# Kernel tuning notes

Measured on AMD Instinct MI355X. Metric: run time of the kernel, lower is better.

Reference implementation:

```python
import jax, jax.numpy as jnp
import numpy as np

B, S, D, H, DH, F = 2, 2048, 768, 12, 64, 3072
EPS = 1e-5


def setup_inputs() -> dict:
    key = jax.random.key(0)
    ks = jax.random.split(key, 12)
    sd = 0.02
    return {
        "x":   jax.random.normal(ks[0], (B, S, D), jnp.float32),
        "Wq":  jax.random.normal(ks[1], (H, D, DH), jnp.float32) * sd,
        "bq":  jnp.zeros((H, DH), jnp.float32),
        "Wk":  jax.random.normal(ks[2], (H, D, DH), jnp.float32) * sd,
        "bk":  jnp.zeros((H, DH), jnp.float32),
        "Wv":  jax.random.normal(ks[3], (H, D, DH), jnp.float32) * sd,
        "bv":  jnp.zeros((H, DH), jnp.float32),
        "Wo":  jax.random.normal(ks[4], (H * DH, D), jnp.float32) * sd,
        "bo":  jnp.zeros((D,), jnp.float32),
        "g1":  jnp.ones((D,), jnp.float32),
        "be1": jnp.zeros((D,), jnp.float32),
        "W1":  jax.random.normal(ks[5], (D, F), jnp.float32) * sd,
        "b1":  jnp.zeros((F,), jnp.float32),
        "W2":  jax.random.normal(ks[6], (F, D), jnp.float32) * sd,
        "b2":  jnp.zeros((D,), jnp.float32),
        "g2":  jnp.ones((D,), jnp.float32),
        "be2": jnp.zeros((D,), jnp.float32),
    }


def _layer_norm(x, g, b):
    mu = jnp.mean(x, axis=-1, keepdims=True)
    var = jnp.mean(jnp.square(x - mu), axis=-1, keepdims=True)
    return (x - mu) * jax.lax.rsqrt(var + EPS) * g + b


def reference(x, Wq, bq, Wk, bk, Wv, bv, Wo, bo, g1, be1, W1, b1, W2, b2, g2, be2):
    # per-head projections (vectorized over heads); eval mode: dropout = identity
    q = jnp.einsum('bsd,hde->bhse', x, Wq) + bq[:, None, :]   # [B,H,S,DH]
    k = jnp.einsum('bsd,hde->bhse', x, Wk) + bk[:, None, :]
    v = jnp.einsum('bsd,hde->bhse', x, Wv) + bv[:, None, :]
    scale = jnp.asarray(DH ** 0.5, x.dtype)
    scores = jnp.einsum('bhse,bhte->bhst', q, k) / scale      # [B,H,S,S]
    attn = jax.nn.softmax(scores, axis=-1)
    ctx = jnp.einsum('bhst,bhte->bhse', attn, v)              # [B,H,S,DH]
    # concat heads (head-major order matches torch.cat over head list)
    concat = jnp.transpose(ctx, (0, 2, 1, 3)).reshape(x.shape[0], x.shape[1], H * DH)
    attn_out = concat @ Wo + bo
    x1 = _layer_norm(x + attn_out, g1, be1)
    ff = jax.nn.relu(x1 @ W1 + b1) @ W2 + b2
    return _layer_norm(x1 + ff, g2, be2)
```

## Files before the change

kernel.cpp:

```cpp
#include <hip/hip_runtime.h>
#include <hip/hip_bf16.h>

typedef __attribute__((ext_vector_type(8))) short short8;
typedef __attribute__((ext_vector_type(4))) float f32x4;

constexpr int Bb  = 2;
constexpr int Ss  = 2048;
constexpr int Dd  = 768;
constexpr int Hh  = 12;
constexpr int DHh = 64;
constexpr int Ff  = 3072;
constexpr int Mr  = Bb * Ss;
constexpr int QKVN = 3 * Hh * DHh;

__device__ __forceinline__ unsigned short f2bf(float f) {
    union { float f; unsigned u; } x{f};
    unsigned r = x.u + 0x7fffu + ((x.u >> 16) & 1u);
    return (unsigned short)(r >> 16);
}

__device__ __forceinline__ int swz(int row, int cbyte) {
    return row * 128 + (cbyte ^ ((row & 7) << 4));
}

__device__ __forceinline__ void gload16(const void* g, void* l) {
    __builtin_amdgcn_global_load_lds(
        (const __attribute__((address_space(1))) unsigned int*)g,
        (__attribute__((address_space(3))) unsigned int*)l, 16, 0, 0);
}

__global__ __launch_bounds__(256) void cast_bf16(const float* __restrict__ in,
                                                 unsigned short* __restrict__ out, int n) {
    int i = (blockIdx.x * 256 + threadIdx.x) * 4;
    if (i >= n) return;
    float4 v = *(const float4*)(in + i);
    ushort4 o;
    o.x = f2bf(v.x); o.y = f2bf(v.y); o.z = f2bf(v.z); o.w = f2bf(v.w);
    *(ushort4*)(out + i) = o;
}

__global__ __launch_bounds__(256) void pack_b(const float* __restrict__ bq,
                                              const float* __restrict__ bk,
                                              const float* __restrict__ bv,
                                              float* __restrict__ bpack) {
    int c = blockIdx.x * 256 + threadIdx.x;
    if (c >= QKVN) return;
    const float* bsrc = (c < 768) ? bq : (c < 1536) ? bk : bv;
    float v = bsrc[c % 768];
    bpack[c] = (c < 768) ? v * 0.125f : v;
}

__global__ __launch_bounds__(256) void transpose_cast_t(const float* __restrict__ W,
                                                        unsigned short* __restrict__ WT,
                                                        int K, int N) {
    __shared__ float t[64][65];
    const int k0 = blockIdx.y * 64, n0 = blockIdx.x * 64;
    const int tid = threadIdx.x;
    const int r = tid >> 4, c4 = (tid & 15) * 4;
#pragma unroll
    for (int i = 0; i < 4; ++i) {
        float4 v = *(const float4*)&W[(size_t)(k0 + r + i * 16) * N + n0 + c4];
        t[r + i * 16][c4 + 0] = v.x;
        t[r + i * 16][c4 + 1] = v.y;
        t[r + i * 16][c4 + 2] = v.z;
        t[r + i * 16][c4 + 3] = v.w;
    }
    __syncthreads();
#pragma unroll
    for (int i = 0; i < 4; ++i) {
        int n = r + i * 16;
        ushort4 o;
        o.x = f2bf(t[c4 + 0][n]);
        o.y = f2bf(t[c4 + 1][n]);
        o.z = f2bf(t[c4 + 2][n]);
        o.w = f2bf(t[c4 + 3][n]);
        *(ushort4*)&WT[(size_t)(n0 + n) * K + k0 + c4] = o;
    }
}

__global__ __launch_bounds__(256) void pack_wqkvT_t(const float* __restrict__ Wq,
                                                    const float* __restrict__ Wk,
                                                    const float* __restrict__ Wv,
                                                    unsigned short* __restrict__ WT) {
    __shared__ float t[64][65];
    const int sh = blockIdx.z;
    const int s = sh / Hh, h = sh % Hh;
    const float* W = ((s == 0) ? Wq : (s == 1) ? Wk : Wv) + (size_t)h * Dd * DHh;
    const float scale = (s == 0) ? 0.125f : 1.0f;
    const int d0 = blockIdx.x * 64;
    const int tid = threadIdx.x;
    const int r = tid >> 4, c4 = (tid & 15) * 4;
#pragma unroll
    for (int i = 0; i < 4; ++i) {
        float4 v = *(const float4*)&W[(size_t)(d0 + r + i * 16) * DHh + c4];
        t[r + i * 16][c4 + 0] = v.x * scale;
        t[r + i * 16][c4 + 1] = v.y * scale;
        t[r + i * 16][c4 + 2] = v.z * scale;
        t[r + i * 16][c4 + 3] = v.w * scale;
    }
    __syncthreads();
    const size_t nbase = (size_t)s * 768 + h * 64;
#pragma unroll
    for (int i = 0; i < 4; ++i) {
        int e = r + i * 16;
        ushort4 o;
        o.x = f2bf(t[c4 + 0][e]);
        o.y = f2bf(t[c4 + 1][e]);
        o.z = f2bf(t[c4 + 2][e]);
        o.w = f2bf(t[c4 + 3][e]);
        *(ushort4*)&WT[(nbase + e) * Dd + d0 + c4] = o;
    }
}

__global__ __launch_bounds__(256) void vtrans(const unsigned short* __restrict__ qkvb,
                                              unsigned short* __restrict__ vT) {
    __shared__ unsigned short t[64][72];
    const int bh = blockIdx.y, b = bh / Hh, h = bh % Hh;
    const int s0 = blockIdx.x * 64;
    const int tid = threadIdx.x;
    for (int i = 0; i < 2; ++i) {
        int slot = i * 256 + tid;
        int r = slot >> 3, c8 = (slot & 7) * 8;
        uint4 v = *(const uint4*)(qkvb + (size_t)(b * Ss + s0 + r) * QKVN + 1536 + h * 64 + c8);
        *(uint4*)&t[r][c8] = v;
    }
    __syncthreads();
    for (int i = 0; i < 2; ++i) {
        int slot = i * 256 + tid;
        int d = slot >> 3, c8 = (slot & 7) * 8;
        alignas(16) unsigned short tmp[8];
#pragma unroll
        for (int j = 0; j < 8; ++j) tmp[j] = t[c8 + j][d];
        *(uint4*)(vT + ((size_t)bh * DHh + d) * Ss + s0 + c8) = *(const uint4*)tmp;
    }
}

template <int OUT_BF16, int RELU>
__global__ __launch_bounds__(256) void gemm_bf16(const unsigned short* __restrict__ A,
                                                 const unsigned short* __restrict__ BT,
                                                 const float* __restrict__ bias,
                                                 void* __restrict__ Cv,
                                                 int M, int N, int K) {
    __shared__ unsigned short As[128 * 32];
    __shared__ unsigned short Bs[128 * 32];
    const int tid = threadIdx.x;
    const int row0 = blockIdx.y * 128, col0 = blockIdx.x * 128;
    const int lane = tid & 63, w = tid >> 6;
    const int wr = w >> 1, wc = w & 1;

    const int ar0 = tid >> 2,         ac0 = (tid & 3) * 8;
    const int ar1 = (tid + 256) >> 2, ac1 = ((tid + 256) & 3) * 8;

    const int kfrag = (lane >> 4) * 8;
    const int rA = wr * 64 + (lane & 15);
    const int rB = wc * 64 + (lane & 15);

    f32x4 acc[4][4] = {};

    for (int k0 = 0; k0 < K; k0 += 32) {
        gload16(&A [(size_t)(row0 + ar0) * K + k0 + ac0], &As[ar0 * 32 + ac0]);
        gload16(&A [(size_t)(row0 + ar1) * K + k0 + ac1], &As[ar1 * 32 + ac1]);
        gload16(&BT[(size_t)(col0 + ar0) * K + k0 + ac0], &Bs[ar0 * 32 + ac0]);
        gload16(&BT[(size_t)(col0 + ar1) * K + k0 + ac1], &Bs[ar1 * 32 + ac1]);
        __syncthreads();

        short8 a[4], b[4];
#pragma unroll
        for (int i = 0; i < 4; ++i) {
            a[i] = *(const short8*)&As[(rA + i * 16) * 32 + kfrag];
            b[i] = *(const short8*)&Bs[(rB + i * 16) * 32 + kfrag];
        }
#pragma unroll
        for (int mi = 0; mi < 4; ++mi)
#pragma unroll
            for (int ni = 0; ni < 4; ++ni)
                acc[mi][ni] = __builtin_amdgcn_mfma_f32_16x16x32_bf16(a[mi], b[ni], acc[mi][ni], 0, 0, 0);
        __syncthreads();
    }

    const int crow = (lane >> 4) * 4, ccol = lane & 15;
#pragma unroll
    for (int mi = 0; mi < 4; ++mi) {
#pragma unroll
        for (int ni = 0; ni < 4; ++ni) {
            const int c = col0 + wc * 64 + ni * 16 + ccol;
            const float bv = bias[c];
#pragma unroll
            for (int j = 0; j < 4; ++j) {
                const int r = row0 + wr * 64 + mi * 16 + crow + j;
                float val = acc[mi][ni][j] + bv;
                if (RELU) val = fmaxf(val, 0.f);
                if (OUT_BF16)
                    ((unsigned short*)Cv)[(size_t)r * N + c] = f2bf(val);
                else
                    ((float*)Cv)[(size_t)r * N + c] = val;
            }
        }
    }
}

__global__ __launch_bounds__(256) void gemm_splitk(const unsigned short* __restrict__ A,
                                                   const unsigned short* __restrict__ BT,
                                                   unsigned short* __restrict__ part,
                                                   int M, int N, int KC, int LD) {
    __shared__ unsigned short As[128 * 32];
    __shared__ unsigned short Bs[128 * 32];
    const int s = blockIdx.z;
    A    += (size_t)s * KC;
    BT   += (size_t)s * KC;
    part += (size_t)s * M * N;

    const int tid = threadIdx.x;
    const int row0 = blockIdx.y * 128, col0 = blockIdx.x * 128;
    const int lane = tid & 63, w = tid >> 6;
    const int wr = w >> 1, wc = w & 1;

    const int ar0 = tid >> 2,         ac0 = (tid & 3) * 8;
    const int ar1 = (tid + 256) >> 2, ac1 = ((tid + 256) & 3) * 8;

    const int kfrag = (lane >> 4) * 8;
    const int rA = wr * 64 + (lane & 15);
    const int rB = wc * 64 + (lane & 15);

    f32x4 acc[4][4] = {};

    for (int k0 = 0; k0 < KC; k0 += 32) {
        gload16(&A [(size_t)(row0 + ar0) * LD + k0 + ac0], &As[ar0 * 32 + ac0]);
        gload16(&A [(size_t)(row0 + ar1) * LD + k0 + ac1], &As[ar1 * 32 + ac1]);
        gload16(&BT[(size_t)(col0 + ar0) * LD + k0 + ac0], &Bs[ar0 * 32 + ac0]);
        gload16(&BT[(size_t)(col0 + ar1) * LD + k0 + ac1], &Bs[ar1 * 32 + ac1]);
        __syncthreads();

        short8 a[4], b[4];
#pragma unroll
        for (int i = 0; i < 4; ++i) {
            a[i] = *(const short8*)&As[(rA + i * 16) * 32 + kfrag];
            b[i] = *(const short8*)&Bs[(rB + i * 16) * 32 + kfrag];
        }
#pragma unroll
        for (int mi = 0; mi < 4; ++mi)
#pragma unroll
            for (int ni = 0; ni < 4; ++ni)
                acc[mi][ni] = __builtin_amdgcn_mfma_f32_16x16x32_bf16(a[mi], b[ni], acc[mi][ni], 0, 0, 0);
        __syncthreads();
    }

    const int crow = (lane >> 4) * 4, ccol = lane & 15;
#pragma unroll
    for (int mi = 0; mi < 4; ++mi)
#pragma unroll
        for (int ni = 0; ni < 4; ++ni) {
            const int c = col0 + wc * 64 + ni * 16 + ccol;
#pragma unroll
            for (int j = 0; j < 4; ++j) {
                const int r = row0 + wr * 64 + mi * 16 + crow + j;
                part[(size_t)r * N + c] = f2bf(acc[mi][ni][j]);
            }
        }
}

template <int S>
__global__ __launch_bounds__(256) void reduce_add(const unsigned short* __restrict__ part,
                                                  const float* __restrict__ bias,
                                                  float* __restrict__ out,
                                                  int N, int MN) {
    int i8 = (blockIdx.x * 256 + threadIdx.x) * 8;
    if (i8 >= MN) return;
    float acc[8] = {};
#pragma unroll
    for (int s = 0; s < S; ++s) {
        short8 v = *(const short8*)(part + (size_t)s * MN + i8);
#pragma unroll
        for (int j = 0; j < 8; ++j) {
            union { unsigned u; float f; } x{(unsigned)(unsigned short)v[j] << 16};
            acc[j] += x.f;
        }
    }
    const int cb = i8 % N;
#pragma unroll
    for (int j = 0; j < 8; ++j) acc[j] += bias[cb + j];
    *(float4*)(out + i8)     = make_float4(acc[0], acc[1], acc[2], acc[3]);
    *(float4*)(out + i8 + 4) = make_float4(acc[4], acc[5], acc[6], acc[7]);
}

__global__ __launch_bounds__(256) void attn_mfma(const unsigned short* __restrict__ qkvb,
                                                 const unsigned short* __restrict__ vT,
                                                 unsigned short* __restrict__ ctx) {
    const int bh = blockIdx.y;
    const int b = bh / Hh, h = bh % Hh;
    const int q0 = blockIdx.x * 64;
    const int tid = threadIdx.x;
    const int lane = tid & 63, w = tid >> 6;

    __shared__ unsigned short Qs[64 * 64];
    __shared__ unsigned short Ks[64 * 64];
    __shared__ unsigned short Vs[64 * 64];
    __shared__ unsigned short Ps[4][16 * 64];

    const unsigned short* qb = qkvb + (size_t)b * Ss * QKVN + h * DHh;

    for (int i = 0; i < 2; ++i) {
        int slot = i * 256 + tid;
        int r = slot >> 3, c8 = (slot & 7) * 8;
        uint4 v = *(const uint4*)(qb + (size_t)(q0 + r) * QKVN + c8);
        *(uint4*)((char*)Qs + swz(r, c8 * 2)) = v;
    }
    __syncthreads();

    short8 qf[2];
#pragma unroll
    for (int kh = 0; kh < 2; ++kh) {
        int r = w * 16 + (lane & 15);
        qf[kh] = *(const short8*)((const char*)Qs + swz(r, kh * 64 + (lane >> 4) * 16));
    }

    float l_[4];
    f32x4 o_[4] = {};
#pragma unroll
    for (int jj = 0; jj < 4; ++jj) l_[jj] = 0.f;

    unsigned short* Pw = &Ps[w][0];

    for (int kt = 0; kt < Ss; kt += 64) {
        __syncthreads();
#pragma unroll
        for (int i = 0; i < 2; ++i) {
            int slot = i * 256 + tid;
            int r = slot >> 3, c8 = (slot & 7) * 8;
            uint4 kv = *(const uint4*)(qb + (size_t)(kt + r) * QKVN + 768 + c8);
            *(uint4*)((char*)Ks + swz(r, c8 * 2)) = kv;
            uint4 vv = *(const uint4*)(vT + ((size_t)bh * DHh + r) * Ss + kt + c8);
            *(uint4*)((char*)Vs + swz(r, c8 * 2)) = vv;
        }
        __syncthreads();

        short8 kf[4][2];
#pragma unroll
        for (int ni = 0; ni < 4; ++ni)
#pragma unroll
            for (int kh = 0; kh < 2; ++kh)
                kf[ni][kh] = *(const short8*)((const char*)Ks + swz(ni * 16 + (lane & 15), kh * 64 + (lane >> 4) * 16));

        f32x4 sa[4] = {};
#pragma unroll
        for (int ni = 0; ni < 4; ++ni) {
            sa[ni] = __builtin_amdgcn_mfma_f32_16x16x32_bf16(qf[0], kf[ni][0], sa[ni], 0, 0, 0);
            sa[ni] = __builtin_amdgcn_mfma_f32_16x16x32_bf16(qf[1], kf[ni][1], sa[ni], 0, 0, 0);
        }

#pragma unroll
        for (int jj = 0; jj < 4; ++jj) {
#pragma unroll
            for (int ni = 0; ni < 4; ++ni) {
                float p = __expf(sa[ni][jj]);
                l_[jj] += p;
                sa[ni][jj] = p;
            }
        }

#pragma unroll
        for (int ni = 0; ni < 4; ++ni)
#pragma unroll
            for (int jj = 0; jj < 4; ++jj) {
                int r = (lane >> 4) * 4 + jj;
                int cb = (ni * 16 + (lane & 15)) * 2;
                *(unsigned short*)((char*)Pw + swz(r, cb)) = f2bf(sa[ni][jj]);
            }

        short8 vf[4][2], pf[2];
#pragma unroll
        for (int di = 0; di < 4; ++di)
#pragma unroll
            for (int kh = 0; kh < 2; ++kh)
                vf[di][kh] = *(const short8*)((const char*)Vs + swz(di * 16 + (lane & 15), kh * 64 + (lane >> 4) * 16));
#pragma unroll
        for (int kh = 0; kh < 2; ++kh)
            pf[kh] = *(const short8*)((const char*)Pw + swz(lane & 15, kh * 64 + (lane >> 4) * 16));
#pragma unroll
        for (int di = 0; di < 4; ++di) {
            o_[di] = __builtin_amdgcn_mfma_f32_16x16x32_bf16(pf[0], vf[di][0], o_[di], 0, 0, 0);
            o_[di] = __builtin_amdgcn_mfma_f32_16x16x32_bf16(pf[1], vf[di][1], o_[di], 0, 0, 0);
        }
    }

    const int crow = (lane >> 4) * 4, ccol = lane & 15;
#pragma unroll
    for (int jj = 0; jj < 4; ++jj) {
        float l = l_[jj];
        l += __shfl_xor(l, 1);
        l += __shfl_xor(l, 2);
        l += __shfl_xor(l, 4);
        l += __shfl_xor(l, 8);
        float inv = 1.f / l;
        int q = q0 + w * 16 + crow + jj;
        unsigned short* orow = ctx + ((size_t)b * Ss + q) * (Hh * DHh) + h * DHh + ccol;
#pragma unroll
        for (int di = 0; di < 4; ++di)
            orow[di * 16] = f2bf(o_[di][jj] * inv);
    }
}

template <int WB16>
__global__ __launch_bounds__(256) void add_ln(const float* __restrict__ a,
                                              const float* __restrict__ bsrc,
                                              const float* __restrict__ g,
                                              const float* __restrict__ be,
                                              float* __restrict__ out,
                                              unsigned short* __restrict__ outb) {
    const int row = blockIdx.x;
    const int tid = threadIdx.x;
    const int lane = tid & 63, wid = tid >> 6;
    __shared__ float red[4];

    const float* pa = a + (size_t)row * Dd;
    const float* pb = bsrc + (size_t)row * Dd;

    float v[3];
    float lsum = 0.f;
#pragma unroll
    for (int i = 0; i < 3; ++i) {
        int idx = tid + i * 256;
        v[i] = pa[idx] + pb[idx];
        lsum += v[i];
    }
#pragma unroll
    for (int o = 32; o > 0; o >>= 1) lsum += __shfl_down(lsum, o);
    if (lane == 0) red[wid] = lsum;
    __syncthreads();
    const float mu = (red[0] + red[1] + red[2] + red[3]) * (1.f / 768.f);

    float lsq = 0.f;
#pragma unroll
    for (int i = 0; i < 3; ++i) {
        float d = v[i] - mu;
        lsq += d * d;
    }
#pragma unroll
    for (int o = 32; o > 0; o >>= 1) lsq += __shfl_down(lsq, o);
    __syncthreads();
    if (lane == 0) red[wid] = lsq;
    __syncthreads();
    const float var = (red[0] + red[1] + red[2] + red[3]) * (1.f / 768.f);
    const float rstd = rsqrtf(var + 1e-5f);

#pragma unroll
    for (int i = 0; i < 3; ++i) {
        int idx = tid + i * 256;
        float o = (v[i] - mu) * rstd * g[idx] + be[idx];
        out[(size_t)row * Dd + idx] = o;
        if (WB16) outb[(size_t)row * Dd + idx] = f2bf(o);
    }
}

extern "C" void kernel_launch(void* const* d_in, const int* in_sizes, int n_in,
                              void* d_out, int out_size, void* d_ws, size_t ws_size,
                              hipStream_t stream) {
    const float* x   = (const float*)d_in[0];
    const float* Wq  = (const float*)d_in[1];
    const float* bq  = (const float*)d_in[2];
    const float* Wk  = (const float*)d_in[3];
    const float* bk  = (const float*)d_in[4];
    const float* Wv  = (const float*)d_in[5];
    const float* bv  = (const float*)d_in[6];
    const float* Wo  = (const float*)d_in[7];
    const float* bo  = (const float*)d_in[8];
    const float* g1  = (const float*)d_in[9];
    const float* be1 = (const float*)d_in[10];
    const float* W1  = (const float*)d_in[11];
    const float* b1  = (const float*)d_in[12];
    const float* W2  = (const float*)d_in[13];
    const float* b2  = (const float*)d_in[14];
    const float* g2  = (const float*)d_in[15];
    const float* be2 = (const float*)d_in[16];
    float* out = (float*)d_out;
    char* ws   = (char*)d_ws;

    unsigned short* qkvb   = (unsigned short*)(ws + 0);
    unsigned short* vT     = (unsigned short*)(ws + 18874368);
    unsigned short* partWo = (unsigned short*)(ws + 0);
    unsigned short* ff1b   = (unsigned short*)(ws + 0);
    float*          ff2out = (float*)        (ws + 0);
    unsigned short* xb     = (unsigned short*)(ws + 25165824);
    unsigned short* WqkvT  = (unsigned short*)(ws + 31457280);
    float*          bpack  = (float*)        (ws + 34996224);
    unsigned short* WoT    = (unsigned short*)(ws + 35005440);
    unsigned short* W1T    = (unsigned short*)(ws + 36185088);
    unsigned short* W2T    = (unsigned short*)(ws + 40903680);
    unsigned short* ctxb   = (unsigned short*)(ws + 45622272);
    float*          attnO  = (float*)        (ws + 51913728);
    unsigned short* partF  = (unsigned short*)(ws + 45622272);
    float*          x1     = (float*)        (ws + 64496640);
    unsigned short* x1b    = (unsigned short*)(ws + 77079552);

    cast_bf16<<<dim3((Mr * Dd / 4 + 255) / 256), 256, 0, stream>>>(x, xb, Mr * Dd);
    pack_wqkvT_t<<<dim3(Dd / 64, 1, 36), 256, 0, stream>>>(Wq, Wk, Wv, WqkvT);
    pack_b<<<dim3(9), 256, 0, stream>>>(bq, bk, bv, bpack);
    transpose_cast_t<<<dim3(Dd / 64, Dd / 64), 256, 0, stream>>>(Wo, WoT, Dd, Dd);
    transpose_cast_t<<<dim3(Ff / 64, Dd / 64), 256, 0, stream>>>(W1, W1T, Dd, Ff);
    transpose_cast_t<<<dim3(Dd / 64, Ff / 64), 256, 0, stream>>>(W2, W2T, Ff, Dd);

    gemm_bf16<1, 0><<<dim3(QKVN / 128, Mr / 128), 256, 0, stream>>>(xb, WqkvT, bpack, qkvb, Mr, QKVN, Dd);

    vtrans<<<dim3(Ss / 64, Bb * Hh), 256, 0, stream>>>(qkvb, vT);

    attn_mfma<<<dim3(Ss / 64, Bb * Hh), 256, 0, stream>>>(qkvb, vT, ctxb);

    gemm_splitk<<<dim3(Dd / 128, Mr / 128, 4), 256, 0, stream>>>(ctxb, WoT, partWo, Mr, Dd, 192, Dd);
    reduce_add<4><<<dim3(Mr * Dd / 8 / 256), 256, 0, stream>>>(partWo, bo, attnO, Dd, Mr * Dd);

    add_ln<1><<<dim3(Mr), 256, 0, stream>>>(x, attnO, g1, be1, x1, x1b);

    gemm_bf16<1, 1><<<dim3(Ff / 128, Mr / 128), 256, 0, stream>>>(x1b, W1T, b1, ff1b, Mr, Ff, Dd);

    gemm_splitk<<<dim3(Dd / 128, Mr / 128, 3), 256, 0, stream>>>(ff1b, W2T, partF, Mr, Dd, 1024, Ff);
    reduce_add<3><<<dim3(Mr * Dd / 8 / 256), 256, 0, stream>>>(partF, b2, ff2out, Dd, Mr * Dd);

    add_ln<0><<<dim3(Mr), 256, 0, stream>>>(x1, ff2out, g2, be2, out, nullptr);
}
```

Baseline: 340.2 us.

## Double-buffer K/V tiles in attention with register prefetch of next tile

The attention kernel now keeps two LDS buffers for K and V. At the start of each iteration it loads the next tile into registers, computes on the current buffer, then writes the prefetched tile into the other buffer. This cuts the loop from two barriers per iteration to one and hides global load latency behind the MFMA and softmax work. In exchange it uses more LDS and more registers, which may lower occupancy.

Result: faster. 320.6 us (-5.7%).

```diff
diff --git a/kernel.cpp b/kernel.cpp
--- a/kernel.cpp
+++ b/kernel.cpp
@@ -293,17 +293,29 @@
     const int lane = tid & 63, w = tid >> 6;
 
     __shared__ unsigned short Qs[64 * 64];
-    __shared__ unsigned short Ks[64 * 64];
-    __shared__ unsigned short Vs[64 * 64];
+    __shared__ unsigned short Ks[2][64 * 64];
+    __shared__ unsigned short Vs[2][64 * 64];
     __shared__ unsigned short Ps[4][16 * 64];
 
     const unsigned short* qb = qkvb + (size_t)b * Ss * QKVN + h * DHh;
-
-    for (int i = 0; i < 2; ++i) {
-        int slot = i * 256 + tid;
-        int r = slot >> 3, c8 = (slot & 7) * 8;
-        uint4 v = *(const uint4*)(qb + (size_t)(q0 + r) * QKVN + c8);
-        *(uint4*)((char*)Qs + swz(r, c8 * 2)) = v;
+    const unsigned short* vb = vT + (size_t)bh * DHh * Ss;
+
+    const int r0 = tid >> 3,         c80 = (tid & 7) * 8;
+    const int r1 = (tid + 256) >> 3, c81 = ((tid + 256) & 7) * 8;
+
+    {
+        uint4 qv0 = *(const uint4*)(qb + (size_t)(q0 + r0) * QKVN + c80);
+        uint4 qv1 = *(const uint4*)(qb + (size_t)(q0 + r1) * QKVN + c81);
+        uint4 kv0 = *(const uint4*)(qb + (size_t)r0 * QKVN + 768 + c80);
+        uint4 kv1 = *(const uint4*)(qb + (size_t)r1 * QKVN + 768 + c81);
+        uint4 vv0 = *(const uint4*)(vb + (size_t)r0 * Ss + c80);
+        uint4 vv1 = *(const uint4*)(vb + (size_t)r1 * Ss + c81);
+        *(uint4*)((char*)Qs + swz(r0, c80 * 2)) = qv0;
+        *(uint4*)((char*)Qs + swz(r1, c81 * 2)) = qv1;
+        *(uint4*)((char*)Ks[0] + swz(r0, c80 * 2)) = kv0;
+        *(uint4*)((char*)Ks[0] + swz(r1, c81 * 2)) = kv1;
+        *(uint4*)((char*)Vs[0] + swz(r0, c80 * 2)) = vv0;
+        *(uint4*)((char*)Vs[0] + swz(r1, c81 * 2)) = vv1;
     }
     __syncthreads();
 
@@ -321,25 +333,25 @@
 
     unsigned short* Pw = &Ps[w][0];
 
-    for (int kt = 0; kt < Ss; kt += 64) {
-        __syncthreads();
-#pragma unroll
-        for (int i = 0; i < 2; ++i) {
-            int slot = i * 256 + tid;
-            int r = slot >> 3, c8 = (slot & 7) * 8;
-            uint4 kv = *(const uint4*)(qb + (size_t)(kt + r) * QKVN + 768 + c8);
-            *(uint4*)((char*)Ks + swz(r, c8 * 2)) = kv;
-            uint4 vv = *(const uint4*)(vT + ((size_t)bh * DHh + r) * Ss + kt + c8);
-            *(uint4*)((char*)Vs + swz(r, c8 * 2)) = vv;
-        }
-        __syncthreads();
+    for (int t = 0; t < Ss / 64; ++t) {
+        const int cur = t & 1, nxt = cur ^ 1;
+        const bool pre = (t < Ss / 64 - 1);
+
+        uint4 kn0, kn1, vn0, vn1;
+        if (pre) {
+            const int kt2 = (t + 1) * 64;
+            kn0 = *(const uint4*)(qb + (size_t)(kt2 + r0) * QKVN + 768 + c80);
+            kn1 = *(const uint4*)(qb + (size_t)(kt2 + r1) * QKVN + 768 + c81);
+            vn0 = *(const uint4*)(vb + (size_t)r0 * Ss + kt2 + c80);
+            vn1 = *(const uint4*)(vb + (size_t)r1 * Ss + kt2 + c81);
+        }
 
         short8 kf[4][2];
 #pragma unroll
         for (int ni = 0; ni < 4; ++ni)
 #pragma unroll
             for (int kh = 0; kh < 2; ++kh)
-                kf[ni][kh] = *(const short8*)((const char*)Ks + swz(ni * 16 + (lane & 15), kh * 64 + (lane >> 4) * 16));
+                kf[ni][kh] = *(const short8*)((const char*)Ks[cur] + swz(ni * 16 + (lane & 15), kh * 64 + (lane >> 4) * 16));
 
         f32x4 sa[4] = {};
 #pragma unroll
@@ -372,7 +384,7 @@
         for (int di = 0; di < 4; ++di)
 #pragma unroll
             for (int kh = 0; kh < 2; ++kh)
-                vf[di][kh] = *(const short8*)((const char*)Vs + swz(di * 16 + (lane & 15), kh * 64 + (lane >> 4) * 16));
+                vf[di][kh] = *(const short8*)((const char*)Vs[cur] + swz(di * 16 + (lane & 15), kh * 64 + (lane >> 4) * 16));
 #pragma unroll
         for (int kh = 0; kh < 2; ++kh)
             pf[kh] = *(const short8*)((const char*)Pw + swz(lane & 15, kh * 64 + (lane >> 4) * 16));
@@ -381,6 +393,14 @@
             o_[di] = __builtin_amdgcn_mfma_f32_16x16x32_bf16(pf[0], vf[di][0], o_[di], 0, 0, 0);
             o_[di] = __builtin_amdgcn_mfma_f32_16x16x32_bf16(pf[1], vf[di][1], o_[di], 0, 0, 0);
         }
+
+        if (pre) {
+            *(uint4*)((char*)Ks[nxt] + swz(r0, c80 * 2)) = kn0;
+            *(uint4*)((char*)Ks[nxt] + swz(r1, c81 * 2)) = kn1;
+            *(uint4*)((char*)Vs[nxt] + swz(r0, c80 * 2)) = vn0;
+            *(uint4*)((char*)Vs[nxt] + swz(r1, c81 * 2)) = vn1;
+        }
+        __syncthreads();
     }
 
     const int crow = (lane >> 4) * 4, ccol = lane & 15;
```
